# Kernel optimization log

Hardware: AMD Instinct MI355X
Metric: run time of the kernel (lower is better)

Reference implementation:

```python
import jax, jax.numpy as jnp
import numpy as np

EPS = 1e-7
BETA = 1.0


def setup_inputs() -> dict:
    key = jax.random.key(0)
    k1, k2, k3, k4 = jax.random.split(key, 4)
    N, E, D_IN, D_OUT = 50000, 800000, 96, 96
    feat = jax.random.normal(k1, (N, D_IN), dtype=jnp.float32)
    src = jax.random.randint(k2, (E,), 0, N, dtype=jnp.int32)
    dst = jax.random.randint(k3, (E,), 0, N, dtype=jnp.int32)
    W = jax.random.normal(k4, (D_IN, D_OUT), dtype=jnp.float32) / np.sqrt(D_IN)
    b = jnp.zeros((D_OUT,), dtype=jnp.float32)
    return {"feat": feat, "src": src, "dst": dst, "W": W, "b": b}


def reference(feat, src, dst, W, b):
    # GENConv with softmax aggregation (canonical DeeperGCN semantics):
    # per edge e=(u,v): m_e = relu(h_u) + eps
    #                   a_e = softmax over edges into v of (beta * m_e)  (per feature dim)
    #                   msg_v = sum_e a_e * m_e
    # out = MLP(h + msg), MLP here = single Linear (mlp_layers=1)
    N = feat.shape[0]
    m = jax.nn.relu(feat[src]) + EPS                     # [E, D]
    logits = BETA * m                                    # [E, D]
    # numerically stable segment softmax over incoming edges of each dst node
    seg_max = jax.ops.segment_max(logits, dst, num_segments=N)   # [N, D]
    ex = jnp.exp(logits - seg_max[dst])                  # [E, D]
    denom = jax.ops.segment_sum(ex, dst, num_segments=N)         # [N, D]
    a = ex / denom[dst]                                  # [E, D]
    msg = jax.ops.segment_sum(a * m, dst, num_segments=N)        # [N, D]
    feats = feat + msg                                   # residual
    return feats @ W + b                                 # [N, D_out]
```

## Files before the change

kernel.cpp:

```cpp
#include <hip/hip_runtime.h>

#define D 96
#define EPSV 1e-7f
#define STRIDE 64
#define NB 32
#define TFUSED 192
#define EPB 2048
#define CAP 5120

__device__ __forceinline__ unsigned short f32_to_bf16_rtne(float x) {
    unsigned int u = __float_as_uint(x);
    u += 0x7fffu + ((u >> 16) & 1u);
    return (unsigned short)(u >> 16);
}
__device__ __forceinline__ float bf16_to_f32(unsigned short u) {
    return __uint_as_float(((unsigned int)u) << 16);
}

__global__ __launch_bounds__(256) void feat_to_bf16(
    const float* __restrict__ feat, ushort* __restrict__ fb, int total4)
{
    int i = blockIdx.x * blockDim.x + threadIdx.x;
    if (i >= total4) return;
    const float4 f = reinterpret_cast<const float4*>(feat)[i];
    ushort4 o;
    o.x = f32_to_bf16_rtne(f.x);
    o.y = f32_to_bf16_rtne(f.y);
    o.z = f32_to_bf16_rtne(f.z);
    o.w = f32_to_bf16_rtne(f.w);
    reinterpret_cast<ushort4*>(fb)[i] = o;
}

__global__ __launch_bounds__(256) void part_pass(
    const int* __restrict__ src, const int* __restrict__ dst,
    uint* __restrict__ cursor,
    uint* __restrict__ stage,
    int E)
{
    __shared__ uint   hist[256];
    __shared__ uint   scn[256];
    __shared__ uint   xbase[256];
    __shared__ uint   gbase[256];
    __shared__ uint   sorted[EPB];
    __shared__ ushort sbid[EPB];

    int t  = threadIdx.x;
    int e0 = blockIdx.x * EPB;
    int tot = E - e0; if (tot > EPB) tot = EPB;

    hist[t] = 0;
    __syncthreads();

    uint myb[EPB / 256], myrk[EPB / 256], myrec[EPB / 256];
    #pragma unroll
    for (int r = 0; r < EPB / 256; ++r) {
        int i = r * 256 + t;
        if (i < tot) {
            int d = dst[e0 + i];
            int s = src[e0 + i];
            uint b = (uint)d >> 8;
            myb[r]  = b;
            myrk[r] = atomicAdd(&hist[b], 1u);
            myrec[r] = (uint)(s & 0xFFFF) | ((uint)(d & 0xFF) << 16);
        }
    }
    __syncthreads();

    scn[t] = hist[t];
    __syncthreads();
    #pragma unroll
    for (int off = 1; off < 256; off <<= 1) {
        uint v = (t >= off) ? scn[t - off] : 0u;
        __syncthreads();
        scn[t] += v;
        __syncthreads();
    }
    xbase[t] = scn[t] - hist[t];
    if (hist[t] > 0)
        gbase[t] = (uint)t * CAP + atomicAdd(&cursor[t], hist[t]);
    __syncthreads();

    #pragma unroll
    for (int r = 0; r < EPB / 256; ++r) {
        int i = r * 256 + t;
        if (i < tot) {
            uint j = xbase[myb[r]] + myrk[r];
            sorted[j] = myrec[r];
            sbid[j]   = (ushort)myb[r];
        }
    }
    __syncthreads();

    #pragma unroll
    for (int r = 0; r < EPB / 256; ++r) {
        int j = r * 256 + t;
        if (j < tot) {
            uint b = sbid[j];
            uint gaddr = gbase[b] + ((uint)j - xbase[b]);
            if (gaddr - b * CAP < CAP)
                stage[gaddr] = sorted[j];
        }
    }
}

__global__ __launch_bounds__(256) void csr_build(
    const uint* __restrict__ cursor, const uint* __restrict__ stage,
    int* __restrict__ deg, ushort* __restrict__ csr, int N)
{
    __shared__ int ldeg[256];
    int b = blockIdx.x;
    int t = threadIdx.x;
    ldeg[t] = 0;
    __syncthreads();

    int cnt = (int)cursor[b]; if (cnt > CAP) cnt = CAP;
    const uint* sp = stage + (size_t)b * CAP;
    for (int i = t; i < cnt; i += 256) {
        uint rec = sp[i];
        int s  = rec & 0xFFFF;
        int dl = (rec >> 16) & 0xFF;
        int slot = atomicAdd(&ldeg[dl], 1);
        if (slot < STRIDE)
            csr[(size_t)((b << 8) + dl) * STRIDE + slot] = (ushort)s;
    }
    __syncthreads();
    int n = (b << 8) + t;
    if (n < N) deg[n] = min(ldeg[t], STRIDE);
}

__global__ __launch_bounds__(256) void build_fast(
    const float* __restrict__ feat, ushort* __restrict__ fb, int total4,
    const int* __restrict__ src, const int* __restrict__ dst,
    int* __restrict__ deg, ushort* __restrict__ csr, int E)
{
    int i = blockIdx.x * 256 + threadIdx.x;
    if (i < total4) {
        const float4 f = reinterpret_cast<const float4*>(feat)[i];
        ushort4 o;
        o.x = f32_to_bf16_rtne(f.x);
        o.y = f32_to_bf16_rtne(f.y);
        o.z = f32_to_bf16_rtne(f.z);
        o.w = f32_to_bf16_rtne(f.w);
        reinterpret_cast<ushort4*>(fb)[i] = o;
    } else {
        int e = i - total4;
        if (e < E) {
            int d = dst[e];
            int pos = atomicAdd(&deg[d], 1);
            if (pos < STRIDE) csr[(size_t)d * STRIDE + pos] = (ushort)src[e];
        }
    }
}

__global__ __launch_bounds__(TFUSED) void fused_gather_gemm(
    const float* __restrict__ feat,
    const ushort* __restrict__ fb,
    const int* __restrict__ degp,
    const ushort* __restrict__ csr,
    const float* __restrict__ W,
    const float* __restrict__ bias,
    float* __restrict__ out,
    int N)
{
    __shared__ float hl[NB][D];

    int t = threadIdx.x;
    int nb0 = blockIdx.x * NB;

    for (int task = t; task < NB * 24; task += TFUSED) {
        int nl = task / 24;
        int q  = (task % 24) * 4;
        int n  = nb0 + nl;
        if (n >= N) continue;

        int beg = n * STRIDE;
        int c = degp[n]; if (c > STRIDE) c = STRIDE;
        int end = beg + c;

        float d0 = 0.f, d1 = 0.f, d2 = 0.f, d3 = 0.f;
        float a0 = 0.f, a1 = 0.f, a2 = 0.f, a3 = 0.f;

        #define PROC(u) { \
            float m0 = fmaxf(bf16_to_f32((u).x), 0.f) + EPSV; \
            float m1 = fmaxf(bf16_to_f32((u).y), 0.f) + EPSV; \
            float m2 = fmaxf(bf16_to_f32((u).z), 0.f) + EPSV; \
            float m3 = fmaxf(bf16_to_f32((u).w), 0.f) + EPSV; \
            float e0 = __expf(m0), e1 = __expf(m1), e2 = __expf(m2), e3 = __expf(m3); \
            d0 += e0; d1 += e1; d2 += e2; d3 += e3; \
            a0 = fmaf(e0, m0, a0); a1 = fmaf(e1, m1, a1); \
            a2 = fmaf(e2, m2, a2); a3 = fmaf(e3, m3, a3); }

        int i = beg;
        for (; i + 4 <= end; i += 4) {
            int s0 = csr[i + 0];
            int s1 = csr[i + 1];
            int s2 = csr[i + 2];
            int s3 = csr[i + 3];
            const ushort4 u0 = *reinterpret_cast<const ushort4*>(fb + (size_t)s0 * D + q);
            const ushort4 u1 = *reinterpret_cast<const ushort4*>(fb + (size_t)s1 * D + q);
            const ushort4 u2 = *reinterpret_cast<const ushort4*>(fb + (size_t)s2 * D + q);
            const ushort4 u3 = *reinterpret_cast<const ushort4*>(fb + (size_t)s3 * D + q);
            PROC(u0); PROC(u1); PROC(u2); PROC(u3);
        }
        for (; i < end; ++i) {
            int s = csr[i];
            const ushort4 u = *reinterpret_cast<const ushort4*>(fb + (size_t)s * D + q);
            PROC(u);
        }
        #undef PROC

        const float4 base = *reinterpret_cast<const float4*>(feat + (size_t)n * D + q);
        bool has = end > beg;
        hl[nl][q + 0] = base.x + (has ? a0 / d0 : 0.f);
        hl[nl][q + 1] = base.y + (has ? a1 / d1 : 0.f);
        hl[nl][q + 2] = base.z + (has ? a2 / d2 : 0.f);
        hl[nl][q + 3] = base.w + (has ? a3 / d3 : 0.f);
    }
    __syncthreads();

    int q   = (t % 24) * 4;
    int grp = t / 24;
    float4 acc0 = *reinterpret_cast<const float4*>(bias + q);
    float4 acc1 = acc0, acc2 = acc0, acc3 = acc0;

    #pragma unroll 4
    for (int k = 0; k < D; ++k) {
        const float4 w = *reinterpret_cast<const float4*>(W + k * D + q);
        float h0 = hl[grp * 4 + 0][k];
        float h1 = hl[grp * 4 + 1][k];
        float h2 = hl[grp * 4 + 2][k];
        float h3 = hl[grp * 4 + 3][k];
        acc0.x = fmaf(h0, w.x, acc0.x); acc0.y = fmaf(h0, w.y, acc0.y);
        acc0.z = fmaf(h0, w.z, acc0.z); acc0.w = fmaf(h0, w.w, acc0.w);
        acc1.x = fmaf(h1, w.x, acc1.x); acc1.y = fmaf(h1, w.y, acc1.y);
        acc1.z = fmaf(h1, w.z, acc1.z); acc1.w = fmaf(h1, w.w, acc1.w);
        acc2.x = fmaf(h2, w.x, acc2.x); acc2.y = fmaf(h2, w.y, acc2.y);
        acc2.z = fmaf(h2, w.z, acc2.z); acc2.w = fmaf(h2, w.w, acc2.w);
        acc3.x = fmaf(h3, w.x, acc3.x); acc3.y = fmaf(h3, w.y, acc3.y);
        acc3.z = fmaf(h3, w.z, acc3.z); acc3.w = fmaf(h3, w.w, acc3.w);
    }

    int n0 = nb0 + grp * 4;
    if (n0 + 0 < N) *reinterpret_cast<float4*>(out + (size_t)(n0 + 0) * D + q) = acc0;
    if (n0 + 1 < N) *reinterpret_cast<float4*>(out + (size_t)(n0 + 1) * D + q) = acc1;
    if (n0 + 2 < N) *reinterpret_cast<float4*>(out + (size_t)(n0 + 2) * D + q) = acc2;
    if (n0 + 3 < N) *reinterpret_cast<float4*>(out + (size_t)(n0 + 3) * D + q) = acc3;
}

extern "C" void kernel_launch(void* const* d_in, const int* in_sizes, int n_in,
                              void* d_out, int out_size, void* d_ws, size_t ws_size,
                              hipStream_t stream) {
    const float* feat = (const float*)d_in[0];
    const int*   src  = (const int*)d_in[1];
    const int*   dst  = (const int*)d_in[2];
    const float* W    = (const float*)d_in[3];
    const float* bias = (const float*)d_in[4];

    int N = in_sizes[0] / D;
    int E = in_sizes[1];
    int total4 = N * D / 4;
    int nbuck  = (N + 255) >> 8;

    size_t fb_bytes    = (size_t)N * D * sizeof(ushort);
    size_t deg_bytes   = (size_t)N * sizeof(int);
    size_t csr_bytes   = (size_t)N * STRIDE * sizeof(ushort);
    size_t cur_bytes   = 256 * sizeof(uint);
    size_t stage_bytes = (size_t)nbuck * CAP * sizeof(uint);

    size_t part_need  = fb_bytes + deg_bytes + csr_bytes + cur_bytes + stage_bytes;
    size_t fast_need  = fb_bytes + deg_bytes + csr_bytes;

    int gblocks = (N + NB - 1) / NB;

    ushort* fb  = (ushort*)d_ws;
    int*    deg = (int*)((char*)d_ws + fb_bytes);
    ushort* csr = (ushort*)((char*)deg + deg_bytes);

    if (ws_size >= part_need) {
        uint* cursor = (uint*)((char*)csr + csr_bytes);
        uint* stage  = (uint*)((char*)cursor + cur_bytes);

        (void)hipMemsetAsync(cursor, 0, cur_bytes, stream);
        feat_to_bf16<<<(total4 + 255) / 256, 256, 0, stream>>>(feat, fb, total4);
        part_pass<<<(E + EPB - 1) / EPB, 256, 0, stream>>>(src, dst, cursor, stage, E);
        csr_build<<<nbuck, 256, 0, stream>>>(cursor, stage, deg, csr, N);
        fused_gather_gemm<<<gblocks, TFUSED, 0, stream>>>(
            feat, fb, deg, csr, W, bias, (float*)d_out, N);
    } else if (ws_size >= fast_need) {
        (void)hipMemsetAsync(deg, 0, deg_bytes, stream);
        int btotal = total4 + E;
        build_fast<<<(btotal + 255) / 256, 256, 0, stream>>>(
            feat, fb, total4, src, dst, deg, csr, E);
        fused_gather_gemm<<<gblocks, TFUSED, 0, stream>>>(
            feat, fb, deg, csr, W, bias, (float*)d_out, N);
    }
}
```

Measured before the change: 96.63 us.

## Merge bf16 conversion into partition kernel and retile fused gather-GEMM

The feature-to-bf16 conversion kernel is folded into the edge-partition kernel as extra blocks, so one launch does both jobs and the two can overlap on the GPU. In the fused gather+GEMM kernel, the nodes per block drop from 32 to 16, which doubles the block count and halves the per-thread row count in the GEMM from 4 to 2. The shared tile is padded to 100 floats per row and read and written as float4 to cut LDS instructions and bank conflicts. The trade-off is that W is now reloaded by twice as many blocks, and the combined kernel carries a blockIdx branch that costs some shared-memory occupancy for the conversion blocks.

```diff
diff --git a/kernel.cpp b/kernel.cpp
--- a/kernel.cpp
+++ b/kernel.cpp
@@ -3,10 +3,11 @@
 #define D 96
 #define EPSV 1e-7f
 #define STRIDE 64
-#define NB 32
+#define NB 16
 #define TFUSED 192
 #define EPB 2048
 #define CAP 5120
+#define HLP 100
 
 __device__ __forceinline__ unsigned short f32_to_bf16_rtne(float x) {
     unsigned int u = __float_as_uint(x);
@@ -17,25 +18,12 @@
     return __uint_as_float(((unsigned int)u) << 16);
 }
 
-__global__ __launch_bounds__(256) void feat_to_bf16(
-    const float* __restrict__ feat, ushort* __restrict__ fb, int total4)
-{
-    int i = blockIdx.x * blockDim.x + threadIdx.x;
-    if (i >= total4) return;
-    const float4 f = reinterpret_cast<const float4*>(feat)[i];
-    ushort4 o;
-    o.x = f32_to_bf16_rtne(f.x);
-    o.y = f32_to_bf16_rtne(f.y);
-    o.z = f32_to_bf16_rtne(f.z);
-    o.w = f32_to_bf16_rtne(f.w);
-    reinterpret_cast<ushort4*>(fb)[i] = o;
-}
-
-__global__ __launch_bounds__(256) void part_pass(
+__global__ __launch_bounds__(256) void part_conv(
     const int* __restrict__ src, const int* __restrict__ dst,
     uint* __restrict__ cursor,
     uint* __restrict__ stage,
-    int E)
+    int E, int pblk,
+    const float* __restrict__ feat, ushort* __restrict__ fb, int total4)
 {
     __shared__ uint   hist[256];
     __shared__ uint   scn[256];
@@ -44,7 +32,22 @@
     __shared__ uint   sorted[EPB];
     __shared__ ushort sbid[EPB];
 
-    int t  = threadIdx.x;
+    int t = threadIdx.x;
+
+    if ((int)blockIdx.x >= pblk) {
+        int i = ((int)blockIdx.x - pblk) * 256 + t;
+        if (i < total4) {
+            const float4 f = reinterpret_cast<const float4*>(feat)[i];
+            ushort4 o;
+            o.x = f32_to_bf16_rtne(f.x);
+            o.y = f32_to_bf16_rtne(f.y);
+            o.z = f32_to_bf16_rtne(f.z);
+            o.w = f32_to_bf16_rtne(f.w);
+            reinterpret_cast<ushort4*>(fb)[i] = o;
+        }
+        return;
+    }
+
     int e0 = blockIdx.x * EPB;
     int tot = E - e0; if (tot > EPB) tot = EPB;
 
@@ -162,7 +165,7 @@
     float* __restrict__ out,
     int N)
 {
-    __shared__ float hl[NB][D];
+    __shared__ float hl[NB][HLP];
 
     int t = threadIdx.x;
     int nb0 = blockIdx.x * NB;
@@ -211,40 +214,50 @@
 
         const float4 base = *reinterpret_cast<const float4*>(feat + (size_t)n * D + q);
         bool has = end > beg;
-        hl[nl][q + 0] = base.x + (has ? a0 / d0 : 0.f);
-        hl[nl][q + 1] = base.y + (has ? a1 / d1 : 0.f);
-        hl[nl][q + 2] = base.z + (has ? a2 / d2 : 0.f);
-        hl[nl][q + 3] = base.w + (has ? a3 / d3 : 0.f);
+        float4 hv;
+        hv.x = base.x + (has ? a0 / d0 : 0.f);
+        hv.y = base.y + (has ? a1 / d1 : 0.f);
+        hv.z = base.z + (has ? a2 / d2 : 0.f);
+        hv.w = base.w + (has ? a3 / d3 : 0.f);
+        *reinterpret_cast<float4*>(&hl[nl][q]) = hv;
     }
     __syncthreads();
 
     int q   = (t % 24) * 4;
     int grp = t / 24;
+    int r0 = grp * 2, r1 = r0 + 1;
     float4 acc0 = *reinterpret_cast<const float4*>(bias + q);
-    float4 acc1 = acc0, acc2 = acc0, acc3 = acc0;
-
-    #pragma unroll 4
-    for (int k = 0; k < D; ++k) {
-        const float4 w = *reinterpret_cast<const float4*>(W + k * D + q);
-        float h0 = hl[grp * 4 + 0][k];
-        float h1 = hl[grp * 4 + 1][k];
-        float h2 = hl[grp * 4 + 2][k];
-        float h3 = hl[grp * 4 + 3][k];
-        acc0.x = fmaf(h0, w.x, acc0.x); acc0.y = fmaf(h0, w.y, acc0.y);
-        acc0.z = fmaf(h0, w.z, acc0.z); acc0.w = fmaf(h0, w.w, acc0.w);
-        acc1.x = fmaf(h1, w.x, acc1.x); acc1.y = fmaf(h1, w.y, acc1.y);
-        acc1.z = fmaf(h1, w.z, acc1.z); acc1.w = fmaf(h1, w.w, acc1.w);
-        acc2.x = fmaf(h2, w.x, acc2.x); acc2.y = fmaf(h2, w.y, acc2.y);
-        acc2.z = fmaf(h2, w.z, acc2.z); acc2.w = fmaf(h2, w.w, acc2.w);
-        acc3.x = fmaf(h3, w.x, acc3.x); acc3.y = fmaf(h3, w.y, acc3.y);
-        acc3.z = fmaf(h3, w.z, acc3.z); acc3.w = fmaf(h3, w.w, acc3.w);
-    }
-
-    int n0 = nb0 + grp * 4;
+    float4 acc1 = acc0;
+
+    #pragma unroll
+    for (int k = 0; k < D; k += 4) {
+        const float4 h0 = *reinterpret_cast<const float4*>(&hl[r0][k]);
+        const float4 h1 = *reinterpret_cast<const float4*>(&hl[r1][k]);
+        const float4 w0 = *reinterpret_cast<const float4*>(W + (k + 0) * D + q);
+        const float4 w1 = *reinterpret_cast<const float4*>(W + (k + 1) * D + q);
+        const float4 w2 = *reinterpret_cast<const float4*>(W + (k + 2) * D + q);
+        const float4 w3 = *reinterpret_cast<const float4*>(W + (k + 3) * D + q);
+        acc0.x = fmaf(h0.x, w0.x, acc0.x); acc0.y = fmaf(h0.x, w0.y, acc0.y);
+        acc0.z = fmaf(h0.x, w0.z, acc0.z); acc0.w = fmaf(h0.x, w0.w, acc0.w);
+        acc0.x = fmaf(h0.y, w1.x, acc0.x); acc0.y = fmaf(h0.y, w1.y, acc0.y);
+        acc0.z = fmaf(h0.y, w1.z, acc0.z); acc0.w = fmaf(h0.y, w1.w, acc0.w);
+        acc0.x = fmaf(h0.z, w2.x, acc0.x); acc0.y = fmaf(h0.z, w2.y, acc0.y);
+        acc0.z = fmaf(h0.z, w2.z, acc0.z); acc0.w = fmaf(h0.z, w2.w, acc0.w);
+        acc0.x = fmaf(h0.w, w3.x, acc0.x); acc0.y = fmaf(h0.w, w3.y, acc0.y);
+        acc0.z = fmaf(h0.w, w3.z, acc0.z); acc0.w = fmaf(h0.w, w3.w, acc0.w);
+        acc1.x = fmaf(h1.x, w0.x, acc1.x); acc1.y = fmaf(h1.x, w0.y, acc1.y);
+        acc1.z = fmaf(h1.x, w0.z, acc1.z); acc1.w = fmaf(h1.x, w0.w, acc1.w);
+        acc1.x = fmaf(h1.y, w1.x, acc1.x); acc1.y = fmaf(h1.y, w1.y, acc1.y);
+        acc1.z = fmaf(h1.y, w1.z, acc1.z); acc1.w = fmaf(h1.y, w1.w, acc1.w);
+        acc1.x = fmaf(h1.z, w2.x, acc1.x); acc1.y = fmaf(h1.z, w2.y, acc1.y);
+        acc1.z = fmaf(h1.z, w2.z, acc1.z); acc1.w = fmaf(h1.z, w2.w, acc1.w);
+        acc1.x = fmaf(h1.w, w3.x, acc1.x); acc1.y = fmaf(h1.w, w3.y, acc1.y);
+        acc1.z = fmaf(h1.w, w3.z, acc1.z); acc1.w = fmaf(h1.w, w3.w, acc1.w);
+    }
+
+    int n0 = nb0 + r0;
     if (n0 + 0 < N) *reinterpret_cast<float4*>(out + (size_t)(n0 + 0) * D + q) = acc0;
     if (n0 + 1 < N) *reinterpret_cast<float4*>(out + (size_t)(n0 + 1) * D + q) = acc1;
-    if (n0 + 2 < N) *reinterpret_cast<float4*>(out + (size_t)(n0 + 2) * D + q) = acc2;
-    if (n0 + 3 < N) *reinterpret_cast<float4*>(out + (size_t)(n0 + 3) * D + q) = acc3;
 }
 
 extern "C" void kernel_launch(void* const* d_in, const int* in_sizes, int n_in,
@@ -280,9 +293,12 @@
         uint* cursor = (uint*)((char*)csr + csr_bytes);
         uint* stage  = (uint*)((char*)cursor + cur_bytes);
 
+        int pblk = (E + EPB - 1) / EPB;
+        int cblk = (total4 + 255) / 256;
+
         (void)hipMemsetAsync(cursor, 0, cur_bytes, stream);
-        feat_to_bf16<<<(total4 + 255) / 256, 256, 0, stream>>>(feat, fb, total4);
-        part_pass<<<(E + EPB - 1) / EPB, 256, 0, stream>>>(src, dst, cursor, stage, E);
+        part_conv<<<pblk + cblk, 256, 0, stream>>>(
+            src, dst, cursor, stage, E, pblk, feat, fb, total4);
         csr_build<<<nbuck, 256, 0, stream>>>(cursor, stage, deg, csr, N);
         fused_gather_gemm<<<gblocks, TFUSED, 0, stream>>>(
             feat, fb, deg, csr, W, bias, (float*)d_out, N);
```

After: 227.0 us. +134.9%, slower.
